# Kernel tuning notes

Hardware: AMD Instinct MI355X
Metric: run time of the kernel (lower is better)

The kernel has to match this reference:

```python
import jax, jax.numpy as jnp
import numpy as np

B, S, H = 2, 512, 768
NH, HD = 12, 64  # num heads, head size


def setup_inputs() -> dict:
    key = jax.random.key(0)
    ks = jax.random.split(key, 11)
    std = 0.02
    return {
        "from_path_hidden": jax.random.normal(ks[0], (B, S, H), jnp.float32),
        "to_path_hidden": jax.random.normal(ks[1], (B, S, H), jnp.float32),
        "attention_mask": jnp.zeros((B, 1, 1, S), jnp.float32),
        "Wq": jax.random.normal(ks[2], (H, H), jnp.float32) * std,
        "bq": jnp.zeros((H,), jnp.float32),
        "Wk": jax.random.normal(ks[3], (H, H), jnp.float32) * std,
        "bk": jnp.zeros((H,), jnp.float32),
        "Wvf": jax.random.normal(ks[4], (H, H), jnp.float32) * std,
        "bvf": jnp.zeros((H,), jnp.float32),
        "Wvt": jax.random.normal(ks[5], (H, H), jnp.float32) * std,
        "bvt": jnp.zeros((H,), jnp.float32),
    }


def _heads(x):
    # [B,S,H] -> [B,NH,S,HD]
    b, s, _ = x.shape
    return x.reshape(b, s, NH, HD).transpose(0, 2, 1, 3)


def reference(from_path_hidden, to_path_hidden, attention_mask,
              Wq, bq, Wk, bk, Wvf, bvf, Wvt, bvt):
    # torch Linear: y = x @ W^T + b
    q = _heads(from_path_hidden @ Wq.T + bq)   # [B,NH,S,HD]
    k = _heads(to_path_hidden @ Wk.T + bk)     # [B,NH,S,HD]
    vf = _heads(from_path_hidden @ Wvf.T + bvf)  # value_from, indexed by query pos
    vt = _heads(to_path_hidden @ Wvt.T + bvt)    # value_to, indexed by key pos

    scores = jnp.einsum("bhqd,bhkd->bhqk", q, k) / jnp.sqrt(jnp.asarray(HD, q.dtype))
    scores = scores + attention_mask  # additive mask, broadcasts [B,1,1,S]
    probs = jax.nn.softmax(scores, axis=-1)  # dropout is identity in eval mode

    # use_expanded_value=True: ctx[b,h,q,:] = sum_k probs[b,h,q,k] * (vf[b,h,q,:] + vt[b,h,k,:])
    # = probs @ vt + (sum_k probs) * vf  -- exact, avoids the [B,NH,S,S,HD] tensor
    ctx = jnp.einsum("bhqk,bhkd->bhqd", probs, vt) + probs.sum(-1, keepdims=True) * vf

    # [B,NH,S,HD] -> [B,S,H]
    ctx = ctx.transpose(0, 2, 1, 3).reshape(from_path_hidden.shape[0], -1, NH * HD)
    return ctx
```

## Files before the change

kernel.cpp:

```cpp
#include <hip/hip_runtime.h>
#include <hip/hip_bf16.h>
#include <math.h>

#define Bq  2
#define Sq  512
#define Hq  768
#define NHq 12
#define HDq 64
#define SHsz (Bq * Sq * Hq)
#define WSZ  (Hq * Hq)

typedef __bf16 bf16x8 __attribute__((ext_vector_type(8)));
typedef unsigned short u16x8 __attribute__((ext_vector_type(8)));
typedef float f32x4 __attribute__((ext_vector_type(4)));

static __device__ __forceinline__ unsigned short f2bf(float f) {
    unsigned int u = __float_as_uint(f);
    u += 0x7fffu + ((u >> 16) & 1u);
    return (unsigned short)(u >> 16);
}
static __device__ __forceinline__ float bf2f(unsigned short v) {
    return __uint_as_float(((unsigned int)v) << 16);
}

static __device__ __forceinline__ f32x4 mfma_bf16(bf16x8 a, bf16x8 b, f32x4 c) {
    return __builtin_amdgcn_mfma_f32_16x16x32_bf16(a, b, c, 0, 0, 0);
}

static __device__ __forceinline__ void async16(const void* g, void* l) {
    __builtin_amdgcn_global_load_lds(
        (const __attribute__((address_space(1))) void*)(uintptr_t)g,
        (__attribute__((address_space(3))) void*)(unsigned int)(uintptr_t)l,
        16, 0, 0);
}

__global__ __launch_bounds__(256) void cvt_kernel(
    const float* __restrict__ from_h, const float* __restrict__ to_h,
    const float* __restrict__ Wq, const float* __restrict__ Wk,
    const float* __restrict__ Wvf, const float* __restrict__ Wvt,
    unsigned short* __restrict__ ws)
{
    const int z = blockIdx.y;
    const float* src; unsigned short* dst; int n;
    switch (z) {
        case 0:  src = from_h; dst = ws + 3 * SHsz;           n = SHsz; break;
        case 1:  src = to_h;   dst = ws + 4 * SHsz;           n = SHsz; break;
        case 2:  src = Wq;     dst = ws + 5 * SHsz;           n = WSZ;  break;
        case 3:  src = Wk;     dst = ws + 5 * SHsz + WSZ;     n = WSZ;  break;
        case 4:  src = Wvf;    dst = ws + 5 * SHsz + 2 * WSZ; n = WSZ;  break;
        default: src = Wvt;    dst = ws + 5 * SHsz + 3 * WSZ; n = WSZ;  break;
    }
    const int idx = (blockIdx.x * 256 + threadIdx.x) * 8;
    if (idx < n) {
        const float4 a = *(const float4*)(src + idx);
        const float4 b = *(const float4*)(src + idx + 4);
        u16x8 o = { f2bf(a.x), f2bf(a.y), f2bf(a.z), f2bf(a.w),
                    f2bf(b.x), f2bf(b.y), f2bf(b.z), f2bf(b.w) };
        *(u16x8*)(dst + idx) = o;
    }
}

__global__ __launch_bounds__(256) void proj_gemm(
    const unsigned short* __restrict__ fbf, const unsigned short* __restrict__ tbf,
    const unsigned short* __restrict__ wqb, const unsigned short* __restrict__ wkb,
    const unsigned short* __restrict__ wvfb, const unsigned short* __restrict__ wvtb,
    const float* __restrict__ bq, const float* __restrict__ bk,
    const float* __restrict__ bvf, const float* __restrict__ bvt,
    unsigned short* __restrict__ qbf, unsigned short* __restrict__ kbf,
    unsigned short* __restrict__ vtt, unsigned short* __restrict__ vfb)
{
    __shared__ unsigned short lds[16384];
    unsigned short* Als = lds;
    unsigned short* Wls = lds + 8192;

    const int z = blockIdx.z;
    const unsigned short *A, *W;
    const float* bias;
    if (z == 0)      { A = fbf; W = wqb;  bias = bq;  }
    else if (z == 1) { A = tbf; W = wkb;  bias = bk;  }
    else if (z == 2) { A = tbf; W = wvtb; bias = bvt; }
    else             { A = fbf; W = wvfb; bias = bvf; }

    const int t    = threadIdx.x;
    const int wv   = t >> 6;
    const int lane = t & 63;
    const int l16  = lane & 15;
    const int quad = lane >> 4;
    const int bn = blockIdx.x;
    const int bm = blockIdx.y;

    const int srow = lane >> 3;
    const int sgrp = (lane & 7) ^ (srow & 7);

    f32x4 acc[4] = {};

    for (int kt = 0; kt < Hq / 128; ++kt) {
        __syncthreads();
        #pragma unroll
        for (int kh = 0; kh < 2; ++kh) {
            const int kc = kt * 128 + kh * 64;
            #pragma unroll
            for (int c = 0; c < 2; ++c) {
                const int r0 = wv * 16 + c * 8;
                async16(A + (size_t)(bm * 64 + r0 + srow) * Hq + kc + sgrp * 8, &Als[kh * 4096 + r0 * 64]);
                async16(W + (size_t)(bn * 64 + r0 + srow) * Hq + kc + sgrp * 8, &Wls[kh * 4096 + r0 * 64]);
            }
        }
        __syncthreads();

        #pragma unroll
        for (int kh = 0; kh < 2; ++kh) {
            #pragma unroll
            for (int kk = 0; kk < 2; ++kk) {
                const int sg = kh * 4096 + ((kk * 4 + quad) ^ (l16 & 7)) * 8;
                const bf16x8 af = *(const bf16x8*)&Als[(wv * 16 + l16) * 64 + sg];
                #pragma unroll
                for (int j = 0; j < 4; ++j) {
                    const bf16x8 bfr = *(const bf16x8*)&Wls[(j * 16 + l16) * 64 + sg];
                    acc[j] = mfma_bf16(af, bfr, acc[j]);
                }
            }
        }
    }

    __syncthreads();

    unsigned short* rep = lds;
    if (z == 2) {
        #pragma unroll
        for (int j = 0; j < 4; ++j) {
            const float bv = bias[bn * 64 + j * 16 + l16];
            #pragma unroll
            for (int r = 0; r < 4; ++r)
                rep[(j * 16 + l16) * 72 + wv * 16 + quad * 4 + r] = f2bf(acc[j][r] + bv);
        }
    } else {
        #pragma unroll
        for (int j = 0; j < 4; ++j) {
            const float bv = bias[bn * 64 + j * 16 + l16];
            #pragma unroll
            for (int r = 0; r < 4; ++r)
                rep[(wv * 16 + quad * 4 + r) * 72 + j * 16 + l16] = f2bf(acc[j][r] + bv);
        }
    }
    __syncthreads();

    const int row = t >> 2;
    #pragma unroll
    for (int p = 0; p < 2; ++p) {
        const int col0 = ((t & 3) + p * 4) * 8;
        const u16x8 v = *(const u16x8*)&rep[row * 72 + col0];
        if (z == 2) {
            const int bb = bm >> 3, m0 = (bm & 7) * 64;
            *(u16x8*)&vtt[((size_t)((bb * NHq + bn) * HDq + row)) * Sq + m0 + col0] = v;
        } else {
            unsigned short* dstp = (z == 0) ? qbf : (z == 1) ? kbf : vfb;
            *(u16x8*)&dstp[(size_t)(bm * 64 + row) * Hq + bn * 64 + col0] = v;
        }
    }
}

__global__ __launch_bounds__(128) void attn_kernel(
    const unsigned short* __restrict__ qbf,
    const unsigned short* __restrict__ kbf,
    const unsigned short* __restrict__ vtt,
    const unsigned short* __restrict__ vfb,
    const float* __restrict__ amask,
    float* __restrict__ outp)
{
    __shared__ unsigned short Plds[2 * 16 * 40];
    __shared__ float Ols[16 * 68];
    __shared__ float Tls[16];

    const int t    = threadIdx.x;
    const int wv   = t >> 6;
    const int lane = t & 63;
    const int l16  = lane & 15;
    const int quad = lane >> 4;
    const int q0 = blockIdx.x * 16;
    const int h  = blockIdx.y;
    const int b  = blockIdx.z;

    const unsigned short* qrow = qbf + ((size_t)(b * Sq + q0 + l16)) * Hq + h * HDq + quad * 8;
    const bf16x8 aq0 = *(const bf16x8*)qrow;
    const bf16x8 aq1 = *(const bf16x8*)(qrow + 32);

    f32x4 O[4] = {};
    float ts[4] = {0.f, 0.f, 0.f, 0.f};
    const float scale = 0.125f;
    unsigned short* myP = &Plds[wv * 16 * 40];

    for (int kt = 0; kt < 8; ++kt) {
        const int k0 = wv * 256 + kt * 32;
        const unsigned short* kr = kbf + ((size_t)(b * Sq + k0 + l16)) * Hq + h * HDq + quad * 8;
        const bf16x8 kb00 = *(const bf16x8*)kr;
        const bf16x8 kb01 = *(const bf16x8*)(kr + 32);
        const bf16x8 kb10 = *(const bf16x8*)(kr + 16 * Hq);
        const bf16x8 kb11 = *(const bf16x8*)(kr + 16 * Hq + 32);

        f32x4 s0 = {}, s1 = {};
        s0 = mfma_bf16(aq0, kb00, s0);
        s0 = mfma_bf16(aq1, kb01, s0);
        s1 = mfma_bf16(aq0, kb10, s1);
        s1 = mfma_bf16(aq1, kb11, s1);

        const float mk0 = amask[b * Sq + k0 + l16];
        const float mk1 = amask[b * Sq + k0 + 16 + l16];

        float p0[4], p1[4];
        #pragma unroll
        for (int r = 0; r < 4; ++r) {
            p0[r] = __expf(s0[r] * scale + mk0);
            p1[r] = __expf(s1[r] * scale + mk1);
            ts[r] += p0[r] + p1[r];
        }

        #pragma unroll
        for (int r = 0; r < 4; ++r) {
            myP[(quad * 4 + r) * 40 + l16]      = f2bf(p0[r]);
            myP[(quad * 4 + r) * 40 + 16 + l16] = f2bf(p1[r]);
        }
        const bf16x8 pa = *(const bf16x8*)&myP[l16 * 40 + quad * 8];

        const unsigned short* vr = vtt + ((size_t)((b * NHq + h) * HDq + l16)) * Sq + k0 + quad * 8;
        #pragma unroll
        for (int j = 0; j < 4; ++j) {
            const bf16x8 vb = *(const bf16x8*)(vr + (size_t)j * 16 * Sq);
            O[j] = mfma_bf16(pa, vb, O[j]);
        }
    }

    #pragma unroll
    for (int off = 1; off < 16; off <<= 1)
        #pragma unroll
        for (int r = 0; r < 4; ++r) ts[r] += __shfl_xor(ts[r], off);

    if (wv == 1) {
        #pragma unroll
        for (int j = 0; j < 4; ++j)
            #pragma unroll
            for (int r = 0; r < 4; ++r)
                Ols[(quad * 4 + r) * 68 + j * 16 + l16] = O[j][r];
        if (l16 == 0)
            #pragma unroll
            for (int r = 0; r < 4; ++r) Tls[quad * 4 + r] = ts[r];
    }
    __syncthreads();
    if (wv == 1) return;

    #pragma unroll
    for (int r = 0; r < 4; ++r) {
        const float inv = 1.f / (ts[r] + Tls[quad * 4 + r]);
        const int row = q0 + quad * 4 + r;
        #pragma unroll
        for (int j = 0; j < 4; ++j) {
            const int col = h * HDq + j * 16 + l16;
            const size_t idx = ((size_t)(b * Sq + row)) * Hq + col;
            const float oj = O[j][r] + Ols[(quad * 4 + r) * 68 + j * 16 + l16];
            outp[idx] = oj * inv + bf2f(vfb[idx]);
        }
    }
}

extern "C" void kernel_launch(void* const* d_in, const int* in_sizes, int n_in,
                              void* d_out, int out_size, void* d_ws, size_t ws_size,
                              hipStream_t stream) {
    (void)in_sizes; (void)n_in; (void)out_size; (void)ws_size;
    const float* from_h = (const float*)d_in[0];
    const float* to_h   = (const float*)d_in[1];
    const float* amask  = (const float*)d_in[2];
    const float* Wq  = (const float*)d_in[3];
    const float* bqv = (const float*)d_in[4];
    const float* Wk  = (const float*)d_in[5];
    const float* bkv = (const float*)d_in[6];
    const float* Wvf = (const float*)d_in[7];
    const float* bvf = (const float*)d_in[8];
    const float* Wvt = (const float*)d_in[9];
    const float* bvt = (const float*)d_in[10];
    float* outp = (float*)d_out;

    unsigned short* ws = (unsigned short*)d_ws;
    unsigned short* qbf = ws;
    unsigned short* kbf = ws + SHsz;
    unsigned short* vtt = ws + 2 * SHsz;
    unsigned short* fbf = ws + 3 * SHsz;
    unsigned short* tbf = ws + 4 * SHsz;
    unsigned short* wqb  = ws + 5 * SHsz;
    unsigned short* wkb  = wqb + WSZ;
    unsigned short* wvfb = wqb + 2 * WSZ;
    unsigned short* wvtb = wqb + 3 * WSZ;
    unsigned short* vfb  = wqb + 4 * WSZ;

    cvt_kernel<<<dim3(384, 6), 256, 0, stream>>>(from_h, to_h, Wq, Wk, Wvf, Wvt, ws);

    dim3 gp(12, 16, 4);
    proj_gemm<<<gp, 256, 0, stream>>>(fbf, tbf, wqb, wkb, wvfb, wvtb,
                                      bqv, bkv, bvf, bvt, qbf, kbf, vtt, vfb);

    dim3 ga(Sq / 16, NHq, Bq);
    attn_kernel<<<ga, 128, 0, stream>>>(qbf, kbf, vtt, vfb, amask, outp);
}
```

Measured before the change: 105.3 us.

## Fuse bf16 conversion into projection GEMM and split attention keys across four waves

Removes the separate fp32-to-bf16 conversion kernel. The projection GEMM now loads fp32 inputs and weights directly and converts them while storing to LDS, replacing the async global-to-LDS copies. The attention kernel uses 256 threads, with each of four waves handling a quarter of the key range; partial outputs and sums are reduced through LDS. This cuts a launch and intermediate memory traffic, but GEMM loads become synchronous and fetch twice the bytes.

```diff
diff --git a/kernel.cpp b/kernel.cpp
--- a/kernel.cpp
+++ b/kernel.cpp
@@ -8,7 +8,6 @@
 #define NHq 12
 #define HDq 64
 #define SHsz (Bq * Sq * Hq)
-#define WSZ  (Hq * Hq)
 
 typedef __bf16 bf16x8 __attribute__((ext_vector_type(8)));
 typedef unsigned short u16x8 __attribute__((ext_vector_type(8)));
@@ -27,43 +26,16 @@
     return __builtin_amdgcn_mfma_f32_16x16x32_bf16(a, b, c, 0, 0, 0);
 }
 
-static __device__ __forceinline__ void async16(const void* g, void* l) {
-    __builtin_amdgcn_global_load_lds(
-        (const __attribute__((address_space(1))) void*)(uintptr_t)g,
-        (__attribute__((address_space(3))) void*)(unsigned int)(uintptr_t)l,
-        16, 0, 0);
-}
-
-__global__ __launch_bounds__(256) void cvt_kernel(
+static __device__ __forceinline__ u16x8 cvt8(float4 a, float4 b) {
+    u16x8 o = { f2bf(a.x), f2bf(a.y), f2bf(a.z), f2bf(a.w),
+                f2bf(b.x), f2bf(b.y), f2bf(b.z), f2bf(b.w) };
+    return o;
+}
+
+__global__ __launch_bounds__(256) void proj_gemm(
     const float* __restrict__ from_h, const float* __restrict__ to_h,
     const float* __restrict__ Wq, const float* __restrict__ Wk,
     const float* __restrict__ Wvf, const float* __restrict__ Wvt,
-    unsigned short* __restrict__ ws)
-{
-    const int z = blockIdx.y;
-    const float* src; unsigned short* dst; int n;
-    switch (z) {
-        case 0:  src = from_h; dst = ws + 3 * SHsz;           n = SHsz; break;
-        case 1:  src = to_h;   dst = ws + 4 * SHsz;           n = SHsz; break;
-        case 2:  src = Wq;     dst = ws + 5 * SHsz;           n = WSZ;  break;
-        case 3:  src = Wk;     dst = ws + 5 * SHsz + WSZ;     n = WSZ;  break;
-        case 4:  src = Wvf;    dst = ws + 5 * SHsz + 2 * WSZ; n = WSZ;  break;
-        default: src = Wvt;    dst = ws + 5 * SHsz + 3 * WSZ; n = WSZ;  break;
-    }
-    const int idx = (blockIdx.x * 256 + threadIdx.x) * 8;
-    if (idx < n) {
-        const float4 a = *(const float4*)(src + idx);
-        const float4 b = *(const float4*)(src + idx + 4);
-        u16x8 o = { f2bf(a.x), f2bf(a.y), f2bf(a.z), f2bf(a.w),
-                    f2bf(b.x), f2bf(b.y), f2bf(b.z), f2bf(b.w) };
-        *(u16x8*)(dst + idx) = o;
-    }
-}
-
-__global__ __launch_bounds__(256) void proj_gemm(
-    const unsigned short* __restrict__ fbf, const unsigned short* __restrict__ tbf,
-    const unsigned short* __restrict__ wqb, const unsigned short* __restrict__ wkb,
-    const unsigned short* __restrict__ wvfb, const unsigned short* __restrict__ wvtb,
     const float* __restrict__ bq, const float* __restrict__ bk,
     const float* __restrict__ bvf, const float* __restrict__ bvt,
     unsigned short* __restrict__ qbf, unsigned short* __restrict__ kbf,
@@ -74,15 +46,15 @@
     unsigned short* Wls = lds + 8192;
 
     const int z = blockIdx.z;
-    const unsigned short *A, *W;
+    const float *A, *W;
     const float* bias;
-    if (z == 0)      { A = fbf; W = wqb;  bias = bq;  }
-    else if (z == 1) { A = tbf; W = wkb;  bias = bk;  }
-    else if (z == 2) { A = tbf; W = wvtb; bias = bvt; }
-    else             { A = fbf; W = wvfb; bias = bvf; }
+    if (z == 0)      { A = from_h; W = Wq;  bias = bq;  }
+    else if (z == 1) { A = to_h;   W = Wk;  bias = bk;  }
+    else if (z == 2) { A = to_h;   W = Wvt; bias = bvt; }
+    else             { A = from_h; W = Wvf; bias = bvf; }
 
     const int t    = threadIdx.x;
-    const int wv   = t >> 6;
+    const int wid  = t >> 6;
     const int lane = t & 63;
     const int l16  = lane & 15;
     const int quad = lane >> 4;
@@ -101,9 +73,15 @@
             const int kc = kt * 128 + kh * 64;
             #pragma unroll
             for (int c = 0; c < 2; ++c) {
-                const int r0 = wv * 16 + c * 8;
-                async16(A + (size_t)(bm * 64 + r0 + srow) * Hq + kc + sgrp * 8, &Als[kh * 4096 + r0 * 64]);
-                async16(W + (size_t)(bn * 64 + r0 + srow) * Hq + kc + sgrp * 8, &Wls[kh * 4096 + r0 * 64]);
+                const int r0 = wid * 16 + c * 8;
+                const size_t ga = (size_t)(bm * 64 + r0 + srow) * Hq + kc + sgrp * 8;
+                const size_t gw = (size_t)(bn * 64 + r0 + srow) * Hq + kc + sgrp * 8;
+                const float4 a0 = *(const float4*)(A + ga);
+                const float4 a1 = *(const float4*)(A + ga + 4);
+                const float4 w0 = *(const float4*)(W + gw);
+                const float4 w1 = *(const float4*)(W + gw + 4);
+                *(u16x8*)&Als[kh * 4096 + r0 * 64 + lane * 8] = cvt8(a0, a1);
+                *(u16x8*)&Wls[kh * 4096 + r0 * 64 + lane * 8] = cvt8(w0, w1);
             }
         }
         __syncthreads();
@@ -113,7 +91,7 @@
             #pragma unroll
             for (int kk = 0; kk < 2; ++kk) {
                 const int sg = kh * 4096 + ((kk * 4 + quad) ^ (l16 & 7)) * 8;
-                const bf16x8 af = *(const bf16x8*)&Als[(wv * 16 + l16) * 64 + sg];
+                const bf16x8 af = *(const bf16x8*)&Als[(wid * 16 + l16) * 64 + sg];
                 #pragma unroll
                 for (int j = 0; j < 4; ++j) {
                     const bf16x8 bfr = *(const bf16x8*)&Wls[(j * 16 + l16) * 64 + sg];
@@ -132,7 +110,7 @@
             const float bv = bias[bn * 64 + j * 16 + l16];
             #pragma unroll
             for (int r = 0; r < 4; ++r)
-                rep[(j * 16 + l16) * 72 + wv * 16 + quad * 4 + r] = f2bf(acc[j][r] + bv);
+                rep[(j * 16 + l16) * 72 + wid * 16 + quad * 4 + r] = f2bf(acc[j][r] + bv);
         }
     } else {
         #pragma unroll
@@ -140,7 +118,7 @@
             const float bv = bias[bn * 64 + j * 16 + l16];
             #pragma unroll
             for (int r = 0; r < 4; ++r)
-                rep[(wv * 16 + quad * 4 + r) * 72 + j * 16 + l16] = f2bf(acc[j][r] + bv);
+                rep[(wid * 16 + quad * 4 + r) * 72 + j * 16 + l16] = f2bf(acc[j][r] + bv);
         }
     }
     __syncthreads();
@@ -160,7 +138,7 @@
     }
 }
 
-__global__ __launch_bounds__(128) void attn_kernel(
+__global__ __launch_bounds__(256) void attn_kernel(
     const unsigned short* __restrict__ qbf,
     const unsigned short* __restrict__ kbf,
     const unsigned short* __restrict__ vtt,
@@ -168,9 +146,9 @@
     const float* __restrict__ amask,
     float* __restrict__ outp)
 {
-    __shared__ unsigned short Plds[2 * 16 * 40];
-    __shared__ float Ols[16 * 68];
-    __shared__ float Tls[16];
+    __shared__ unsigned short Plds[4 * 16 * 40];
+    __shared__ float Ols[3 * 16 * 68];
+    __shared__ float Tls[3 * 16];
 
     const int t    = threadIdx.x;
     const int wv   = t >> 6;
@@ -190,8 +168,8 @@
     const float scale = 0.125f;
     unsigned short* myP = &Plds[wv * 16 * 40];
 
-    for (int kt = 0; kt < 8; ++kt) {
-        const int k0 = wv * 256 + kt * 32;
+    for (int kt = 0; kt < 4; ++kt) {
+        const int k0 = wv * 128 + kt * 32;
         const unsigned short* kr = kbf + ((size_t)(b * Sq + k0 + l16)) * Hq + h * HDq + quad * 8;
         const bf16x8 kb00 = *(const bf16x8*)kr;
         const bf16x8 kb01 = *(const bf16x8*)(kr + 32);
@@ -235,28 +213,34 @@
         #pragma unroll
         for (int r = 0; r < 4; ++r) ts[r] += __shfl_xor(ts[r], off);
 
-    if (wv == 1) {
+    if (wv > 0) {
+        float* myO = &Ols[(wv - 1) * 16 * 68];
         #pragma unroll
         for (int j = 0; j < 4; ++j)
             #pragma unroll
             for (int r = 0; r < 4; ++r)
-                Ols[(quad * 4 + r) * 68 + j * 16 + l16] = O[j][r];
+                myO[(quad * 4 + r) * 68 + j * 16 + l16] = O[j][r];
         if (l16 == 0)
             #pragma unroll
-            for (int r = 0; r < 4; ++r) Tls[quad * 4 + r] = ts[r];
+            for (int r = 0; r < 4; ++r) Tls[(wv - 1) * 16 + quad * 4 + r] = ts[r];
     }
     __syncthreads();
-    if (wv == 1) return;
+    if (wv > 0) return;
 
     #pragma unroll
     for (int r = 0; r < 4; ++r) {
-        const float inv = 1.f / (ts[r] + Tls[quad * 4 + r]);
-        const int row = q0 + quad * 4 + r;
+        const int rr = quad * 4 + r;
+        const float tot = ts[r] + Tls[rr] + Tls[16 + rr] + Tls[32 + rr];
+        const float inv = 1.f / tot;
+        const int row = q0 + rr;
         #pragma unroll
         for (int j = 0; j < 4; ++j) {
             const int col = h * HDq + j * 16 + l16;
             const size_t idx = ((size_t)(b * Sq + row)) * Hq + col;
-            const float oj = O[j][r] + Ols[(quad * 4 + r) * 68 + j * 16 + l16];
+            const float oj = O[j][r]
+                + Ols[rr * 68 + j * 16 + l16]
+                + Ols[16 * 68 + rr * 68 + j * 16 + l16]
+                + Ols[2 * 16 * 68 + rr * 68 + j * 16 + l16];
             outp[idx] = oj * inv + bf2f(vfb[idx]);
         }
     }
@@ -283,20 +267,12 @@
     unsigned short* qbf = ws;
     unsigned short* kbf = ws + SHsz;
     unsigned short* vtt = ws + 2 * SHsz;
-    unsigned short* fbf = ws + 3 * SHsz;
-    unsigned short* tbf = ws + 4 * SHsz;
-    unsigned short* wqb  = ws + 5 * SHsz;
-    unsigned short* wkb  = wqb + WSZ;
-    unsigned short* wvfb = wqb + 2 * WSZ;
-    unsigned short* wvtb = wqb + 3 * WSZ;
-    unsigned short* vfb  = wqb + 4 * WSZ;
-
-    cvt_kernel<<<dim3(384, 6), 256, 0, stream>>>(from_h, to_h, Wq, Wk, Wvf, Wvt, ws);
+    unsigned short* vfb = ws + 3 * SHsz;
 
     dim3 gp(12, 16, 4);
-    proj_gemm<<<gp, 256, 0, stream>>>(fbf, tbf, wqb, wkb, wvfb, wvtb,
+    proj_gemm<<<gp, 256, 0, stream>>>(from_h, to_h, Wq, Wk, Wvf, Wvt,
                                       bqv, bkv, bvf, bvt, qbf, kbf, vtt, vfb);
 
     dim3 ga(Sq / 16, NHq, Bq);
-    attn_kernel<<<ga, 128, 0, stream>>>(qbf, kbf, vtt, vfb, amask, outp);
-}
+    attn_kernel<<<ga, 256, 0, stream>>>(qbf, kbf, vtt, vfb, amask, outp);
+}
```

After: 117.1 us. 1.11x slower.
